# Kernel tuning notes

Measured on AMD Instinct MI355X. Metric: run time of the kernel, lower is better.

## Reference

```python
import jax, jax.numpy as jnp
import numpy as np

STATE_DIM = 64
HIDDEN_DIM = 256
BATCH = 4096
DT = 0.01


def setup_inputs() -> dict:
    key = jax.random.key(0)
    ks = jax.random.split(key, 7)
    s = 1.0 / np.sqrt(STATE_DIM)
    h = 1.0 / np.sqrt(HIDDEN_DIM)
    return {
        "x0": jax.random.normal(ks[0], (BATCH, STATE_DIM), dtype=jnp.float32),
        "W1": jax.random.uniform(ks[1], (STATE_DIM, HIDDEN_DIM), jnp.float32, -s, s),
        "b1": jax.random.uniform(ks[2], (HIDDEN_DIM,), jnp.float32, -s, s),
        "W2": jax.random.uniform(ks[3], (HIDDEN_DIM, HIDDEN_DIM), jnp.float32, -h, h),
        "b2": jax.random.uniform(ks[4], (HIDDEN_DIM,), jnp.float32, -h, h),
        "W3": jax.random.uniform(ks[5], (HIDDEN_DIM, STATE_DIM), jnp.float32, -h, h),
        "b3": jax.random.uniform(ks[6], (STATE_DIM,), jnp.float32, -h, h),
        "dt_scale": jnp.ones((1,), dtype=jnp.float32) * 0.01,
        "steps": 200,
    }


def reference(x0, W1, b1, W2, b2, W3, b3, dt_scale, steps):
    def func(x):
        h1 = jnp.tanh(x @ W1 + b1)
        h2 = jnp.tanh(h1 @ W2 + b2)
        return h2 @ W3 + b3

    def step(x, _):
        x_next = x + func(x) * dt_scale * DT  # Euler update
        return x_next, x_next

    _, traj = jax.lax.scan(step, x0, None, length=steps)
    # traj: [steps, batch, state_dim] -> [batch, steps+1, state_dim]
    return jnp.concatenate([x0[:, None, :], jnp.swapaxes(traj, 0, 1)], axis=1)
```

## Files before the change

### kernel.cpp

```cpp
#include <hip/hip_runtime.h>


#define STATE_DIM 64
#define HIDDEN    256
#define TILE_M    16
#define NBLK      256
#define XPITCH    68
#define HPITCH    260

typedef short v8s __attribute__((ext_vector_type(8)));
typedef float v4f __attribute__((ext_vector_type(4)));

__device__ __forceinline__ unsigned short f2bf(float f) {
    return (unsigned short)((__float_as_uint(f) + 0x8000u) >> 16);
}
__device__ __forceinline__ unsigned pk2bf(float a, float b) {
    return ((__float_as_uint(a) + 0x8000u) >> 16) |
           ((__float_as_uint(b) + 0x8000u) & 0xffff0000u);
}
__device__ __forceinline__ float fast_tanh(float x) {
    float e = __builtin_amdgcn_exp2f(x * 2.8853900817779268f);
    return 1.0f - 2.0f * __builtin_amdgcn_rcpf(e + 1.0f);
}

__global__ void prep_weights(const float* __restrict__ W1,
                             const float* __restrict__ W2,
                             const float* __restrict__ W3,
                             short* __restrict__ W1t,
                             short* __restrict__ W2t,
                             short* __restrict__ W3t) {
    int u = blockIdx.x * 256 + threadIdx.x;
    if (u < 65536) {
        int n = u >> 8, k = u & 255;
        W2t[u] = (short)f2bf(W2[k * 256 + n]);
    }
    int v = u - 65536;
    if (v >= 0 && v < 16384) {
        int n = v >> 6, k = v & 63;
        W1t[v] = (short)f2bf(W1[k * 256 + n]);
    }
    int t = u - (65536 + 16384);
    if (t >= 0 && t < 16384) {
        int n = t >> 8, k = t & 255;
        W3t[t] = (short)f2bf(W3[k * 64 + n]);
    }
}

__global__ __launch_bounds__(512, 2)
void ode_kernel(const float* __restrict__ x0,
                const float* __restrict__ b1,
                const float* __restrict__ b2,
                const float* __restrict__ b3,
                const float* __restrict__ dt_scale,
                const int*   __restrict__ stepsp,
                const short* __restrict__ W1t,
                const short* __restrict__ W2t,
                const short* __restrict__ W3t,
                float* __restrict__ out) {
    __shared__ short xb [TILE_M * XPITCH];
    __shared__ short h1b[TILE_M * HPITCH];
    __shared__ short h2b[TILE_M * HPITCH];

    const int tid  = threadIdx.x;
    const int w    = tid >> 6;
    const int lane = tid & 63;
    const int ln   = lane & 15;
    const int q    = lane >> 4;
    const int blk  = blockIdx.x;
    const int nsteps = *stepsp;
    const float scale = dt_scale[0] * 0.01f;
    const int n0 = 32 * w;

    v8s w1f[2][2], w2f[2][8], w3f[8];
    #pragma unroll
    for (int t = 0; t < 2; t++)
        #pragma unroll
        for (int ks = 0; ks < 2; ks++)
            w1f[t][ks] = *(const v8s*)(W1t + (n0 + 16 * t + ln) * 64 + 32 * ks + 8 * q);
    #pragma unroll
    for (int t = 0; t < 2; t++)
        #pragma unroll
        for (int ks = 0; ks < 8; ks++)
            w2f[t][ks] = *(const v8s*)(W2t + (n0 + 16 * t + ln) * 256 + 32 * ks + 8 * q);
    if (w < 4) {
        #pragma unroll
        for (int ks = 0; ks < 8; ks++)
            w3f[ks] = *(const v8s*)(W3t + (16 * w + ln) * 256 + 32 * ks + 8 * q);
    }
    v4f b1v[2], b2v[2], b3v = {0.f, 0.f, 0.f, 0.f};
    #pragma unroll
    for (int t = 0; t < 2; t++) {
        b1v[t] = *(const v4f*)(b1 + n0 + 16 * t + 4 * q);
        b2v[t] = *(const v4f*)(b2 + n0 + 16 * t + 4 * q);
    }
    if (w < 4) b3v = *(const v4f*)(b3 + 16 * w + 4 * q);

    v4f x = {0.f, 0.f, 0.f, 0.f};
    unsigned tbase = 0;
    const int xw0 = ln * XPITCH + 16 * w + 4 * q;
    if (w < 4) {
        x = *(const v4f*)(x0 + (size_t)(blk * TILE_M + ln) * STATE_DIM + 16 * w + 4 * q);
        uint2 p; p.x = pk2bf(x[0], x[1]); p.y = pk2bf(x[2], x[3]);
        *(uint2*)(xb + xw0) = p;
        tbase = (unsigned)(blk * TILE_M + ln) * (unsigned)((nsteps + 1) * STATE_DIM)
              + 16 * w + 4 * q;
        *(v4f*)(out + tbase) = x;
        tbase += STATE_DIM;
    }
    __syncthreads();

    int xrd[2], hrd[8];
    #pragma unroll
    for (int ks = 0; ks < 2; ks++) xrd[ks] = ln * XPITCH + 32 * ks + 8 * q;
    #pragma unroll
    for (int ks = 0; ks < 8; ks++) hrd[ks] = ln * HPITCH + 32 * ks + 8 * q;
    const int hw0 = ln * HPITCH + n0 + 4 * q;

    for (int s = 0; s < nsteps; s++) {
        v8s xa0 = *(const v8s*)(xb + xrd[0]);
        v8s xa1 = *(const v8s*)(xb + xrd[1]);
        v4f a0 = b1v[0], a1 = b1v[1];
        a0 = __builtin_amdgcn_mfma_f32_16x16x32_bf16(w1f[0][0], xa0, a0, 0, 0, 0);
        a1 = __builtin_amdgcn_mfma_f32_16x16x32_bf16(w1f[1][0], xa0, a1, 0, 0, 0);
        a0 = __builtin_amdgcn_mfma_f32_16x16x32_bf16(w1f[0][1], xa1, a0, 0, 0, 0);
        a1 = __builtin_amdgcn_mfma_f32_16x16x32_bf16(w1f[1][1], xa1, a1, 0, 0, 0);
        {
            uint2 p0, p1;
            p0.x = pk2bf(fast_tanh(a0[0]), fast_tanh(a0[1]));
            p0.y = pk2bf(fast_tanh(a0[2]), fast_tanh(a0[3]));
            p1.x = pk2bf(fast_tanh(a1[0]), fast_tanh(a1[1]));
            p1.y = pk2bf(fast_tanh(a1[2]), fast_tanh(a1[3]));
            *(uint2*)(h1b + hw0)      = p0;
            *(uint2*)(h1b + hw0 + 16) = p1;
        }
        __syncthreads();

        v8s ha[8];
        #pragma unroll
        for (int ks = 0; ks < 8; ks++) ha[ks] = *(const v8s*)(h1b + hrd[ks]);
        a0 = b2v[0]; a1 = b2v[1];
        #pragma unroll
        for (int ks = 0; ks < 8; ks++) {
            a0 = __builtin_amdgcn_mfma_f32_16x16x32_bf16(w2f[0][ks], ha[ks], a0, 0, 0, 0);
            a1 = __builtin_amdgcn_mfma_f32_16x16x32_bf16(w2f[1][ks], ha[ks], a1, 0, 0, 0);
        }
        {
            uint2 p0, p1;
            p0.x = pk2bf(fast_tanh(a0[0]), fast_tanh(a0[1]));
            p0.y = pk2bf(fast_tanh(a0[2]), fast_tanh(a0[3]));
            p1.x = pk2bf(fast_tanh(a1[0]), fast_tanh(a1[1]));
            p1.y = pk2bf(fast_tanh(a1[2]), fast_tanh(a1[3]));
            *(uint2*)(h2b + hw0)      = p0;
            *(uint2*)(h2b + hw0 + 16) = p1;
        }
        __syncthreads();

        if (w < 4) {
            v8s hc[8];
            #pragma unroll
            for (int ks = 0; ks < 8; ks++) hc[ks] = *(const v8s*)(h2b + hrd[ks]);
            v4f a3 = b3v;
            #pragma unroll
            for (int ks = 0; ks < 8; ks++)
                a3 = __builtin_amdgcn_mfma_f32_16x16x32_bf16(w3f[ks], hc[ks], a3, 0, 0, 0);
            #pragma unroll
            for (int i = 0; i < 4; i++)
                x[i] = fmaf(a3[i], scale, x[i]);
            uint2 p; p.x = pk2bf(x[0], x[1]); p.y = pk2bf(x[2], x[3]);
            *(uint2*)(xb + xw0) = p;
            *(v4f*)(out + tbase) = x;
            tbase += STATE_DIM;
        }
        __syncthreads();
    }
}

extern "C" void kernel_launch(void* const* d_in, const int* in_sizes, int n_in,
                              void* d_out, int out_size, void* d_ws, size_t ws_size,
                              hipStream_t stream) {
    const float* x0 = (const float*)d_in[0];
    const float* W1 = (const float*)d_in[1];
    const float* b1 = (const float*)d_in[2];
    const float* W2 = (const float*)d_in[3];
    const float* b2 = (const float*)d_in[4];
    const float* W3 = (const float*)d_in[5];
    const float* b3 = (const float*)d_in[6];
    const float* dt = (const float*)d_in[7];
    const int* steps = (const int*)d_in[8];

    short* W1t = (short*)d_ws;
    short* W2t = W1t + 64 * 256;
    short* W3t = W2t + 256 * 256;

    prep_weights<<<384, 256, 0, stream>>>(W1, W2, W3, W1t, W2t, W3t);
    ode_kernel<<<NBLK, 512, 0, stream>>>(x0, b1, b2, b3, dt, steps,
                                         W1t, W2t, W3t, (float*)d_out);
}
```

Before: 429.3 us.

## Fold W3 into W1 to propagate pre-activation z and drop one barrier per step

Precomputes W31 = W3·W1·scale and its bias, so each step carries the layer-1 pre-activation z forward in fp32 as z += h2·W31 + bW1s. This removes the per-step x round trip through LDS and the third barrier, leaving two barriers per step. The x update moves to the upper warps, and the reductions are split into two accumulator chains. The packed bf16 conversion now uses a single hardware instruction. The cost is a doubled K=256 MFMA workload for layer-1 work, more weight registers, and a slightly different rounding path, since z no longer comes from a bf16-quantized x.

```diff
diff --git a/kernel.cpp b/kernel.cpp
--- a/kernel.cpp
+++ b/kernel.cpp
@@ -1,12 +1,10 @@
 #include <hip/hip_runtime.h>
 
 
-#define STATE_DIM 64
-#define HIDDEN    256
-#define TILE_M    16
-#define NBLK      256
-#define XPITCH    68
-#define HPITCH    260
+#define TILE_M 16
+#define NBLK   256
+#define XPITCH 68
+#define HPITCH 260
 
 typedef short v8s __attribute__((ext_vector_type(8)));
 typedef float v4f __attribute__((ext_vector_type(4)));
@@ -14,21 +12,28 @@
 __device__ __forceinline__ unsigned short f2bf(float f) {
     return (unsigned short)((__float_as_uint(f) + 0x8000u) >> 16);
 }
-__device__ __forceinline__ unsigned pk2bf(float a, float b) {
-    return ((__float_as_uint(a) + 0x8000u) >> 16) |
-           ((__float_as_uint(b) + 0x8000u) & 0xffff0000u);
+__device__ __forceinline__ unsigned cvt_pk_bf16(float a, float b) {
+    unsigned r;
+    asm("v_cvt_pk_bf16_f32 %0, %1, %2" : "=v"(r) : "v"(a), "v"(b));
+    return r;
 }
 __device__ __forceinline__ float fast_tanh(float x) {
     float e = __builtin_amdgcn_exp2f(x * 2.8853900817779268f);
     return 1.0f - 2.0f * __builtin_amdgcn_rcpf(e + 1.0f);
 }
+__device__ __forceinline__ void sync_lds() {
+    asm volatile("s_waitcnt lgkmcnt(0)" ::: "memory");
+    __builtin_amdgcn_s_barrier();
+    asm volatile("" ::: "memory");
+}
 
 __global__ void prep_weights(const float* __restrict__ W1,
                              const float* __restrict__ W2,
                              const float* __restrict__ W3,
+                             const float* __restrict__ dt_scale,
                              short* __restrict__ W1t,
                              short* __restrict__ W2t,
-                             short* __restrict__ W3t) {
+                             short* __restrict__ W3ts) {
     int u = blockIdx.x * 256 + threadIdx.x;
     if (u < 65536) {
         int n = u >> 8, k = u & 255;
@@ -41,8 +46,33 @@
     }
     int t = u - (65536 + 16384);
     if (t >= 0 && t < 16384) {
+        float scale = dt_scale[0] * 0.01f;
         int n = t >> 8, k = t & 255;
-        W3t[t] = (short)f2bf(W3[k * 64 + n]);
+        W3ts[t] = (short)f2bf(W3[k * 64 + n] * scale);
+    }
+}
+
+__global__ void prep_w31(const float* __restrict__ W1,
+                         const float* __restrict__ W3,
+                         const float* __restrict__ b3,
+                         const float* __restrict__ dt_scale,
+                         short* __restrict__ W31t,
+                         float* __restrict__ bW1s) {
+    int k = blockIdx.x;
+    int n = threadIdx.x;
+    float scale = dt_scale[0] * 0.01f;
+    if (k < 256) {
+        float acc = 0.f;
+        #pragma unroll 8
+        for (int j = 0; j < 64; j++)
+            acc = fmaf(W3[k * 64 + j], W1[j * 256 + n], acc);
+        W31t[n * 256 + k] = (short)f2bf(acc * scale);
+    } else {
+        float acc = 0.f;
+        #pragma unroll 8
+        for (int j = 0; j < 64; j++)
+            acc = fmaf(b3[j], W1[j * 256 + n], acc);
+        bW1s[n] = acc * scale;
     }
 }
 
@@ -55,11 +85,13 @@
                 const int*   __restrict__ stepsp,
                 const short* __restrict__ W1t,
                 const short* __restrict__ W2t,
-                const short* __restrict__ W3t,
+                const short* __restrict__ W3ts,
+                const short* __restrict__ W31t,
+                const float* __restrict__ bW1s,
                 float* __restrict__ out) {
-    __shared__ short xb [TILE_M * XPITCH];
     __shared__ short h1b[TILE_M * HPITCH];
     __shared__ short h2b[TILE_M * HPITCH];
+    __shared__ short xb [TILE_M * XPITCH];
 
     const int tid  = threadIdx.x;
     const int w    = tid >> 6;
@@ -68,110 +100,142 @@
     const int q    = lane >> 4;
     const int blk  = blockIdx.x;
     const int nsteps = *stepsp;
-    const float scale = dt_scale[0] * 0.01f;
     const int n0 = 32 * w;
-
-    v8s w1f[2][2], w2f[2][8], w3f[8];
+    const bool xw = (w >= 4);
+    const int t3 = w & 3;
+
+    v8s w2f[2][8], w31f[2][8], w3f[8];
     #pragma unroll
     for (int t = 0; t < 2; t++)
         #pragma unroll
-        for (int ks = 0; ks < 2; ks++)
-            w1f[t][ks] = *(const v8s*)(W1t + (n0 + 16 * t + ln) * 64 + 32 * ks + 8 * q);
-    #pragma unroll
-    for (int t = 0; t < 2; t++)
+        for (int ks = 0; ks < 8; ks++) {
+            w2f [t][ks] = *(const v8s*)(W2t  + (n0 + 16 * t + ln) * 256 + 32 * ks + 8 * q);
+            w31f[t][ks] = *(const v8s*)(W31t + (n0 + 16 * t + ln) * 256 + 32 * ks + 8 * q);
+        }
+    if (xw) {
         #pragma unroll
         for (int ks = 0; ks < 8; ks++)
-            w2f[t][ks] = *(const v8s*)(W2t + (n0 + 16 * t + ln) * 256 + 32 * ks + 8 * q);
-    if (w < 4) {
-        #pragma unroll
-        for (int ks = 0; ks < 8; ks++)
-            w3f[ks] = *(const v8s*)(W3t + (16 * w + ln) * 256 + 32 * ks + 8 * q);
-    }
-    v4f b1v[2], b2v[2], b3v = {0.f, 0.f, 0.f, 0.f};
+            w3f[ks] = *(const v8s*)(W3ts + (16 * t3 + ln) * 256 + 32 * ks + 8 * q);
+    }
+
+    v4f b2v[2], bzv[2], b3s = {0.f, 0.f, 0.f, 0.f};
     #pragma unroll
     for (int t = 0; t < 2; t++) {
-        b1v[t] = *(const v4f*)(b1 + n0 + 16 * t + 4 * q);
-        b2v[t] = *(const v4f*)(b2 + n0 + 16 * t + 4 * q);
-    }
-    if (w < 4) b3v = *(const v4f*)(b3 + 16 * w + 4 * q);
+        b2v[t] = *(const v4f*)(b2   + n0 + 16 * t + 4 * q);
+        bzv[t] = *(const v4f*)(bW1s + n0 + 16 * t + 4 * q);
+    }
+    const float scale = dt_scale[0] * 0.01f;
+    if (xw) {
+        v4f bt = *(const v4f*)(b3 + 16 * t3 + 4 * q);
+        b3s = bt * scale;
+    }
 
     v4f x = {0.f, 0.f, 0.f, 0.f};
     unsigned tbase = 0;
-    const int xw0 = ln * XPITCH + 16 * w + 4 * q;
-    if (w < 4) {
-        x = *(const v4f*)(x0 + (size_t)(blk * TILE_M + ln) * STATE_DIM + 16 * w + 4 * q);
-        uint2 p; p.x = pk2bf(x[0], x[1]); p.y = pk2bf(x[2], x[3]);
-        *(uint2*)(xb + xw0) = p;
-        tbase = (unsigned)(blk * TILE_M + ln) * (unsigned)((nsteps + 1) * STATE_DIM)
-              + 16 * w + 4 * q;
+    if (xw) {
+        x = *(const v4f*)(x0 + (size_t)(blk * TILE_M + ln) * 64 + 16 * t3 + 4 * q);
+        uint2 p; p.x = cvt_pk_bf16(x[0], x[1]); p.y = cvt_pk_bf16(x[2], x[3]);
+        *(uint2*)(xb + ln * XPITCH + 16 * t3 + 4 * q) = p;
+        tbase = (unsigned)(blk * TILE_M + ln) * (unsigned)((nsteps + 1) * 64)
+              + 16 * t3 + 4 * q;
         *(v4f*)(out + tbase) = x;
-        tbase += STATE_DIM;
-    }
-    __syncthreads();
-
-    int xrd[2], hrd[8];
-    #pragma unroll
-    for (int ks = 0; ks < 2; ks++) xrd[ks] = ln * XPITCH + 32 * ks + 8 * q;
-    #pragma unroll
-    for (int ks = 0; ks < 8; ks++) hrd[ks] = ln * HPITCH + 32 * ks + 8 * q;
-    const int hw0 = ln * HPITCH + n0 + 4 * q;
+        tbase += 64;
+    }
+    sync_lds();
+
+    v4f z0, z1;
+    {
+        v8s xa0 = *(const v8s*)(xb + ln * XPITCH + 8 * q);
+        v8s xa1 = *(const v8s*)(xb + ln * XPITCH + 32 + 8 * q);
+        v8s w1a[2][2];
+        #pragma unroll
+        for (int t = 0; t < 2; t++)
+            #pragma unroll
+            for (int ks = 0; ks < 2; ks++)
+                w1a[t][ks] = *(const v8s*)(W1t + (n0 + 16 * t + ln) * 64 + 32 * ks + 8 * q);
+        z0 = *(const v4f*)(b1 + n0 + 4 * q);
+        z1 = *(const v4f*)(b1 + n0 + 16 + 4 * q);
+        z0 = __builtin_amdgcn_mfma_f32_16x16x32_bf16(w1a[0][0], xa0, z0, 0, 0, 0);
+        z1 = __builtin_amdgcn_mfma_f32_16x16x32_bf16(w1a[1][0], xa0, z1, 0, 0, 0);
+        z0 = __builtin_amdgcn_mfma_f32_16x16x32_bf16(w1a[0][1], xa1, z0, 0, 0, 0);
+        z1 = __builtin_amdgcn_mfma_f32_16x16x32_bf16(w1a[1][1], xa1, z1, 0, 0, 0);
+    }
+
+    const short* hr1 = h1b + ln * HPITCH + 8 * q;
+    const short* hr2 = h2b + ln * HPITCH + 8 * q;
+    short* hw1 = h1b + ln * HPITCH + n0 + 4 * q;
+    short* hw2 = h2b + ln * HPITCH + n0 + 4 * q;
+
+    {
+        uint2 p0, p1;
+        p0.x = cvt_pk_bf16(fast_tanh(z0[0]), fast_tanh(z0[1]));
+        p0.y = cvt_pk_bf16(fast_tanh(z0[2]), fast_tanh(z0[3]));
+        p1.x = cvt_pk_bf16(fast_tanh(z1[0]), fast_tanh(z1[1]));
+        p1.y = cvt_pk_bf16(fast_tanh(z1[2]), fast_tanh(z1[3]));
+        *(uint2*)(hw1)      = p0;
+        *(uint2*)(hw1 + 16) = p1;
+    }
+    sync_lds();
 
     for (int s = 0; s < nsteps; s++) {
-        v8s xa0 = *(const v8s*)(xb + xrd[0]);
-        v8s xa1 = *(const v8s*)(xb + xrd[1]);
-        v4f a0 = b1v[0], a1 = b1v[1];
-        a0 = __builtin_amdgcn_mfma_f32_16x16x32_bf16(w1f[0][0], xa0, a0, 0, 0, 0);
-        a1 = __builtin_amdgcn_mfma_f32_16x16x32_bf16(w1f[1][0], xa0, a1, 0, 0, 0);
-        a0 = __builtin_amdgcn_mfma_f32_16x16x32_bf16(w1f[0][1], xa1, a0, 0, 0, 0);
-        a1 = __builtin_amdgcn_mfma_f32_16x16x32_bf16(w1f[1][1], xa1, a1, 0, 0, 0);
+        v8s ha[8];
+        #pragma unroll
+        for (int ks = 0; ks < 8; ks++) ha[ks] = *(const v8s*)(hr1 + 32 * ks);
+        v4f a0 = b2v[0], a1 = b2v[1];
+        v4f c0 = {0.f, 0.f, 0.f, 0.f}, c1 = {0.f, 0.f, 0.f, 0.f};
+        #pragma unroll
+        for (int ks = 0; ks < 4; ks++) {
+            a0 = __builtin_amdgcn_mfma_f32_16x16x32_bf16(w2f[0][ks],     ha[ks],     a0, 0, 0, 0);
+            a1 = __builtin_amdgcn_mfma_f32_16x16x32_bf16(w2f[1][ks],     ha[ks],     a1, 0, 0, 0);
+            c0 = __builtin_amdgcn_mfma_f32_16x16x32_bf16(w2f[0][ks + 4], ha[ks + 4], c0, 0, 0, 0);
+            c1 = __builtin_amdgcn_mfma_f32_16x16x32_bf16(w2f[1][ks + 4], ha[ks + 4], c1, 0, 0, 0);
+        }
+        a0 += c0; a1 += c1;
         {
             uint2 p0, p1;
-            p0.x = pk2bf(fast_tanh(a0[0]), fast_tanh(a0[1]));
-            p0.y = pk2bf(fast_tanh(a0[2]), fast_tanh(a0[3]));
-            p1.x = pk2bf(fast_tanh(a1[0]), fast_tanh(a1[1]));
-            p1.y = pk2bf(fast_tanh(a1[2]), fast_tanh(a1[3]));
-            *(uint2*)(h1b + hw0)      = p0;
-            *(uint2*)(h1b + hw0 + 16) = p1;
-        }
-        __syncthreads();
-
-        v8s ha[8];
-        #pragma unroll
-        for (int ks = 0; ks < 8; ks++) ha[ks] = *(const v8s*)(h1b + hrd[ks]);
-        a0 = b2v[0]; a1 = b2v[1];
-        #pragma unroll
-        for (int ks = 0; ks < 8; ks++) {
-            a0 = __builtin_amdgcn_mfma_f32_16x16x32_bf16(w2f[0][ks], ha[ks], a0, 0, 0, 0);
-            a1 = __builtin_amdgcn_mfma_f32_16x16x32_bf16(w2f[1][ks], ha[ks], a1, 0, 0, 0);
-        }
+            p0.x = cvt_pk_bf16(fast_tanh(a0[0]), fast_tanh(a0[1]));
+            p0.y = cvt_pk_bf16(fast_tanh(a0[2]), fast_tanh(a0[3]));
+            p1.x = cvt_pk_bf16(fast_tanh(a1[0]), fast_tanh(a1[1]));
+            p1.y = cvt_pk_bf16(fast_tanh(a1[2]), fast_tanh(a1[3]));
+            *(uint2*)(hw2)      = p0;
+            *(uint2*)(hw2 + 16) = p1;
+        }
+        sync_lds();
+
+        v8s hc[8];
+        #pragma unroll
+        for (int ks = 0; ks < 8; ks++) hc[ks] = *(const v8s*)(hr2 + 32 * ks);
+        v4f p0 = bzv[0], p1 = bzv[1];
+        #pragma unroll
+        for (int ks = 0; ks < 4; ks++) {
+            z0 = __builtin_amdgcn_mfma_f32_16x16x32_bf16(w31f[0][ks],     hc[ks],     z0, 0, 0, 0);
+            z1 = __builtin_amdgcn_mfma_f32_16x16x32_bf16(w31f[1][ks],     hc[ks],     z1, 0, 0, 0);
+            p0 = __builtin_amdgcn_mfma_f32_16x16x32_bf16(w31f[0][ks + 4], hc[ks + 4], p0, 0, 0, 0);
+            p1 = __builtin_amdgcn_mfma_f32_16x16x32_bf16(w31f[1][ks + 4], hc[ks + 4], p1, 0, 0, 0);
+        }
+        z0 += p0; z1 += p1;
+        if (xw) {
+            v4f xa = x, xc = b3s;
+            #pragma unroll
+            for (int ks = 0; ks < 4; ks++) {
+                xa = __builtin_amdgcn_mfma_f32_16x16x32_bf16(w3f[ks],     hc[ks],     xa, 0, 0, 0);
+                xc = __builtin_amdgcn_mfma_f32_16x16x32_bf16(w3f[ks + 4], hc[ks + 4], xc, 0, 0, 0);
+            }
+            x = xa + xc;
+            *(v4f*)(out + tbase) = x;
+            tbase += 64;
+        }
+
         {
-            uint2 p0, p1;
-            p0.x = pk2bf(fast_tanh(a0[0]), fast_tanh(a0[1]));
-            p0.y = pk2bf(fast_tanh(a0[2]), fast_tanh(a0[3]));
-            p1.x = pk2bf(fast_tanh(a1[0]), fast_tanh(a1[1]));
-            p1.y = pk2bf(fast_tanh(a1[2]), fast_tanh(a1[3]));
-            *(uint2*)(h2b + hw0)      = p0;
-            *(uint2*)(h2b + hw0 + 16) = p1;
-        }
-        __syncthreads();
-
-        if (w < 4) {
-            v8s hc[8];
-            #pragma unroll
-            for (int ks = 0; ks < 8; ks++) hc[ks] = *(const v8s*)(h2b + hrd[ks]);
-            v4f a3 = b3v;
-            #pragma unroll
-            for (int ks = 0; ks < 8; ks++)
-                a3 = __builtin_amdgcn_mfma_f32_16x16x32_bf16(w3f[ks], hc[ks], a3, 0, 0, 0);
-            #pragma unroll
-            for (int i = 0; i < 4; i++)
-                x[i] = fmaf(a3[i], scale, x[i]);
-            uint2 p; p.x = pk2bf(x[0], x[1]); p.y = pk2bf(x[2], x[3]);
-            *(uint2*)(xb + xw0) = p;
-            *(v4f*)(out + tbase) = x;
-            tbase += STATE_DIM;
-        }
-        __syncthreads();
+            uint2 q0, q1;
+            q0.x = cvt_pk_bf16(fast_tanh(z0[0]), fast_tanh(z0[1]));
+            q0.y = cvt_pk_bf16(fast_tanh(z0[2]), fast_tanh(z0[3]));
+            q1.x = cvt_pk_bf16(fast_tanh(z1[0]), fast_tanh(z1[1]));
+            q1.y = cvt_pk_bf16(fast_tanh(z1[2]), fast_tanh(z1[3]));
+            *(uint2*)(hw1)      = q0;
+            *(uint2*)(hw1 + 16) = q1;
+        }
+        sync_lds();
     }
 }
 
@@ -188,11 +252,15 @@
     const float* dt = (const float*)d_in[7];
     const int* steps = (const int*)d_in[8];
 
-    short* W1t = (short*)d_ws;
-    short* W2t = W1t + 64 * 256;
-    short* W3t = W2t + 256 * 256;
-
-    prep_weights<<<384, 256, 0, stream>>>(W1, W2, W3, W1t, W2t, W3t);
+    short* W1t  = (short*)d_ws;
+    short* W2t  = W1t + 64 * 256;
+    short* W3ts = W2t + 256 * 256;
+    short* W31t = W3ts + 64 * 256;
+    float* bW1s = (float*)(W31t + 256 * 256);
+
+    prep_weights<<<384, 256, 0, stream>>>(W1, W2, W3, dt, W1t, W2t, W3ts);
+    prep_w31<<<257, 256, 0, stream>>>(W1, W3, b3, dt, W31t, bW1s);
     ode_kernel<<<NBLK, 512, 0, stream>>>(x0, b1, b2, b3, dt, steps,
-                                         W1t, W2t, W3t, (float*)d_out);
-}
+                                         W1t, W2t, W3ts, W31t, bW1s,
+                                         (float*)d_out);
+}
```

Measured after the change: 991.7 us. +131.0%, slower.

## Stage trajectory in LDS for batched flushes and split MFMA accumulation chains

Applied to the files above, without the earlier changes.

Each step's new state is written into a 4-slot shared-memory ring instead of being stored straight to global memory. Every fourth step, all 512 threads write four consecutive step rows to global memory as contiguous 1 KB runs per batch row, with a tail flush for leftover steps. The layer-2 and layer-3 MFMA reductions are also split into two independent accumulator chains that are summed at the end, which shortens the dependent MFMA latency chain. The cost is extra LDS traffic plus a flush phase every four steps, and the changed summation order may shift rounding slightly.

```diff
diff --git a/kernel.cpp b/kernel.cpp
--- a/kernel.cpp
+++ b/kernel.cpp
@@ -7,6 +7,7 @@
 #define NBLK      256
 #define XPITCH    68
 #define HPITCH    260
+#define TPITCH    68
 
 typedef short v8s __attribute__((ext_vector_type(8)));
 typedef float v4f __attribute__((ext_vector_type(4)));
@@ -60,6 +61,7 @@
     __shared__ short xb [TILE_M * XPITCH];
     __shared__ short h1b[TILE_M * HPITCH];
     __shared__ short h2b[TILE_M * HPITCH];
+    __shared__ float tb [4][TILE_M][TPITCH];
 
     const int tid  = threadIdx.x;
     const int w    = tid >> 6;
@@ -95,17 +97,23 @@
     }
     if (w < 4) b3v = *(const v4f*)(b3 + 16 * w + 4 * q);
 
+    const unsigned ns1x64 = (unsigned)(nsteps + 1) * 64u;
+    const int fr = tid >> 5;
+    const int fu = tid & 31;
+    const int fk = fu >> 3;
+    const int ff = (fu & 7) * 8;
+    const unsigned gflush = (unsigned)(blk * TILE_M + fr) * ns1x64
+                          + (unsigned)(fk + 1) * 64u + (unsigned)ff;
+    const float* trd = &tb[fk][fr][ff];
+
     v4f x = {0.f, 0.f, 0.f, 0.f};
-    unsigned tbase = 0;
     const int xw0 = ln * XPITCH + 16 * w + 4 * q;
     if (w < 4) {
         x = *(const v4f*)(x0 + (size_t)(blk * TILE_M + ln) * STATE_DIM + 16 * w + 4 * q);
         uint2 p; p.x = pk2bf(x[0], x[1]); p.y = pk2bf(x[2], x[3]);
         *(uint2*)(xb + xw0) = p;
-        tbase = (unsigned)(blk * TILE_M + ln) * (unsigned)((nsteps + 1) * STATE_DIM)
-              + 16 * w + 4 * q;
-        *(v4f*)(out + tbase) = x;
-        tbase += STATE_DIM;
+        unsigned t0 = (unsigned)(blk * TILE_M + ln) * ns1x64 + 16 * w + 4 * q;
+        *(v4f*)(out + t0) = x;
     }
     __syncthreads();
 
@@ -139,11 +147,15 @@
         #pragma unroll
         for (int ks = 0; ks < 8; ks++) ha[ks] = *(const v8s*)(h1b + hrd[ks]);
         a0 = b2v[0]; a1 = b2v[1];
-        #pragma unroll
-        for (int ks = 0; ks < 8; ks++) {
-            a0 = __builtin_amdgcn_mfma_f32_16x16x32_bf16(w2f[0][ks], ha[ks], a0, 0, 0, 0);
-            a1 = __builtin_amdgcn_mfma_f32_16x16x32_bf16(w2f[1][ks], ha[ks], a1, 0, 0, 0);
-        }
+        v4f c0 = {0.f, 0.f, 0.f, 0.f}, c1 = {0.f, 0.f, 0.f, 0.f};
+        #pragma unroll
+        for (int ks = 0; ks < 4; ks++) {
+            a0 = __builtin_amdgcn_mfma_f32_16x16x32_bf16(w2f[0][ks],     ha[ks],     a0, 0, 0, 0);
+            a1 = __builtin_amdgcn_mfma_f32_16x16x32_bf16(w2f[1][ks],     ha[ks],     a1, 0, 0, 0);
+            c0 = __builtin_amdgcn_mfma_f32_16x16x32_bf16(w2f[0][ks + 4], ha[ks + 4], c0, 0, 0, 0);
+            c1 = __builtin_amdgcn_mfma_f32_16x16x32_bf16(w2f[1][ks + 4], ha[ks + 4], c1, 0, 0, 0);
+        }
+        a0 += c0; a1 += c1;
         {
             uint2 p0, p1;
             p0.x = pk2bf(fast_tanh(a0[0]), fast_tanh(a0[1]));
@@ -160,18 +172,37 @@
             #pragma unroll
             for (int ks = 0; ks < 8; ks++) hc[ks] = *(const v8s*)(h2b + hrd[ks]);
             v4f a3 = b3v;
+            v4f c3 = {0.f, 0.f, 0.f, 0.f};
             #pragma unroll
-            for (int ks = 0; ks < 8; ks++)
-                a3 = __builtin_amdgcn_mfma_f32_16x16x32_bf16(w3f[ks], hc[ks], a3, 0, 0, 0);
+            for (int ks = 0; ks < 4; ks++) {
+                a3 = __builtin_amdgcn_mfma_f32_16x16x32_bf16(w3f[ks],     hc[ks],     a3, 0, 0, 0);
+                c3 = __builtin_amdgcn_mfma_f32_16x16x32_bf16(w3f[ks + 4], hc[ks + 4], c3, 0, 0, 0);
+            }
             #pragma unroll
             for (int i = 0; i < 4; i++)
-                x[i] = fmaf(a3[i], scale, x[i]);
+                x[i] = fmaf(a3[i] + c3[i], scale, x[i]);
             uint2 p; p.x = pk2bf(x[0], x[1]); p.y = pk2bf(x[2], x[3]);
             *(uint2*)(xb + xw0) = p;
-            *(v4f*)(out + tbase) = x;
-            tbase += STATE_DIM;
+            *(v4f*)(&tb[s & 3][ln][16 * w + 4 * q]) = x;
         }
         __syncthreads();
+
+        if ((s & 3) == 3) {
+            v4f d0 = *(const v4f*)(trd);
+            v4f d1 = *(const v4f*)(trd + 4);
+            unsigned ga = gflush + (unsigned)(s - 3) * 64u;
+            *(v4f*)(out + ga)     = d0;
+            *(v4f*)(out + ga + 4) = d1;
+        }
+    }
+
+    int rem = nsteps & 3;
+    if (rem && fk < rem) {
+        v4f d0 = *(const v4f*)(trd);
+        v4f d1 = *(const v4f*)(trd + 4);
+        unsigned ga = gflush + (unsigned)(nsteps - rem) * 64u;
+        *(v4f*)(out + ga)     = d0;
+        *(v4f*)(out + ga + 4) = d1;
     }
 }
 
```

After: 454.7 us. 1.06x slower.
